# Kernel optimization log

Hardware: AMD Instinct MI355X
Metric: run time of the kernel (lower is better)

Reference implementation:

```python
import jax, jax.numpy as jnp
import numpy as np


def _conv2d_valid(x, w):
    # x: (N, C, H, W), w: (O, C, kH, kW) -> (N, O, H-kH+1, W-kW+1)
    return jax.lax.conv_general_dilated(
        x, w, window_strides=(1, 1), padding='VALID',
        dimension_numbers=('NCHW', 'OIHW', 'NCHW'))


def setup_inputs() -> dict:
    key = jax.random.key(0)
    kx, ky = jax.random.split(key)
    x = jax.random.normal(kx, (16, 64, 128, 128), dtype=jnp.float32)
    y = jax.random.normal(ky, (64, 64, 16, 16), dtype=jnp.float32)
    return {"x": x, "y": y}


def reference(x, y):
    # Normalize each of the K kernels to unit L2 norm (sum over C, kH, kW).
    normed_y = y / jnp.sqrt(jnp.sum(y * y, axis=(1, 2, 3), keepdims=True))
    # Per-window L2 norm of x via ones-kernel box conv over x^2.
    ones_kernel = jnp.ones(y.shape, dtype=x.dtype)
    x_norm = jnp.sqrt(_conv2d_valid(x * x, ones_kernel))
    # Normalized cross-correlation, clamped at zero.
    diss = _conv2d_valid(x, normed_y) / x_norm
    return jax.nn.relu(diss)
```

## Files before the change

### kernel.cpp

```cpp
#include <hip/hip_runtime.h>
#include <stdint.h>

#define GAS __attribute__((address_space(1)))
#define LAS __attribute__((address_space(3)))

typedef __attribute__((ext_vector_type(8))) short short8;
typedef __attribute__((ext_vector_type(4))) float float4v;
typedef __attribute__((ext_vector_type(4))) unsigned int uint4v;

__device__ __forceinline__ unsigned short f2bf(float f) {
  union { float f; unsigned int u; } v; v.f = f;
  unsigned int r = v.u + 0x7fffu + ((v.u >> 16) & 1u);
  return (unsigned short)(r >> 16);
}

__device__ __forceinline__ void async_g2l16(const void* g, void* l) {
  __builtin_amdgcn_global_load_lds((const GAS unsigned int*)g,
                                   (LAS unsigned int*)l, 16, 0, 0);
}

__device__ __forceinline__ void vmem_drain() {
  asm volatile("s_waitcnt vmcnt(0)" ::: "memory");
}

__global__ void knorm_y(const float* __restrict__ y, unsigned short* __restrict__ y_t2) {
  int o = blockIdx.x;
  int tid = threadIdx.x;
  const float* yo = y + o * 16384;
  float s = 0.f;
  for (int idx = tid; idx < 16384; idx += 256) { float v = yo[idx]; s += v * v; }
  for (int off = 32; off; off >>= 1) s += __shfl_down(s, off, 64);
  __shared__ float red[4];
  if ((tid & 63) == 0) red[tid >> 6] = s;
  __syncthreads();
  float rn = 1.0f / sqrtf(red[0] + red[1] + red[2] + red[3]);
  int og = o >> 4, ol = o & 15;
  for (int idx = tid; idx < 16384; idx += 256) {
    int c = idx >> 8, dy = (idx >> 4) & 15, dx = idx & 15;
    int t = dy * 16 + dx;
    int cb = c >> 5, q = (c >> 3) & 3, j = c & 7;
    size_t dst = (size_t)t * 4096 + (size_t)(og * 2 + cb) * 512 + (q * 16 + ol) * 8 + j;
    y_t2[dst] = f2bf(yo[idx] * rn);
  }
}

__global__ void ktrans_x(const float* __restrict__ x, unsigned short* __restrict__ x_t,
                         float* __restrict__ s) {
  int h = blockIdx.x, n = blockIdx.y;
  int tid = threadIdx.x;
  __shared__ __align__(16) unsigned short tb[8192];
  __shared__ float sb[256];
  const float* xb = x + ((size_t)n * 64) * 16384 + h * 128;
  int w = tid & 127, half = tid >> 7;
  float acc = 0.f;
#pragma unroll
  for (int cs = 0; cs < 4; ++cs) {
    short8 tmp;
#pragma unroll
    for (int j = 0; j < 8; ++j) {
      int c = half * 32 + cs * 8 + j;
      float v = xb[(size_t)c * 16384 + w];
      tmp[j] = (short)f2bf(v);
      acc += v * v;
    }
    int chunk = (half * 4 + cs) ^ (w & 7);
    *(short8*)(tb + w * 64 + chunk * 8) = tmp;
  }
  sb[tid] = acc;
  __syncthreads();
  uint4v* dst = (uint4v*)(x_t + ((size_t)(n * 128 + h)) * 8192);
  const uint4v* src = (const uint4v*)tb;
  for (int idx = tid; idx < 1024; idx += 256) dst[idx] = src[idx];
  if (tid < 128) s[((size_t)(n * 128 + h)) * 128 + tid] = sb[tid] + sb[tid + 128];
}

__global__ void knorm_x(const float* __restrict__ s, float* __restrict__ invn) {
  int i = blockIdx.x, n = blockIdx.y;
  int tid = threadIdx.x;
  __shared__ float colsum[128];
  const float* sp = s + ((size_t)(n * 128 + i)) * 128;
  float a = 0.f;
#pragma unroll
  for (int dy = 0; dy < 16; ++dy) a += sp[dy * 128 + tid];
  colsum[tid] = a;
  __syncthreads();
  if (tid < 113) {
    float acc = 0.f;
#pragma unroll
    for (int dx = 0; dx < 16; ++dx) acc += colsum[tid + dx];
    invn[((size_t)n * 113 + i) * 113 + tid] = 1.0f / sqrtf(acc);
  }
}

__launch_bounds__(256, 3)
__global__ void kconv(const unsigned short* __restrict__ x_t,
                      const unsigned short* __restrict__ y_t2,
                      const float* __restrict__ invn,
                      float* __restrict__ out) {
  int i = blockIdx.x;
  int n = blockIdx.y;
  int tid = threadIdx.x;
  int lane = tid & 63, wave = tid >> 6;
  int lane15 = lane & 15, q = lane >> 4;
  int wrow = wave >> 1, wcol = wave & 1;

  __shared__ __align__(16) char smem[32768];
  char* const A0 = smem;
  char* const A1 = smem + 16384;

  const char* xrow0 = (const char*)(x_t + ((size_t)(n * 128 + i)) * 8192);

  auto stageA = [&](int dy, char* buf) {
    const char* src = xrow0 + (size_t)dy * 16384;
#pragma unroll
    for (int it = 0; it < 4; ++it) {
      int chunk = it * 256 + wave * 64;
      async_g2l16(src + (chunk + lane) * 16, buf + chunk * 16);
    }
  };

  const short8* ybase = (const short8*)(y_t2 + (size_t)wcol * 2048 + (size_t)lane * 8);
  auto loadB = [&](int t, short8 bf[2][2]) {
    const short8* p = ybase + (size_t)t * 512;
    bf[0][0] = p[0];
    bf[0][1] = p[64];
    bf[1][0] = p[128];
    bf[1][1] = p[192];
  };

  float4v acc[4][2];
#pragma unroll
  for (int mt = 0; mt < 4; ++mt)
#pragma unroll
    for (int nt = 0; nt < 2; ++nt) acc[mt][nt] = (float4v){0.f, 0.f, 0.f, 0.f};

  int abase[4];
#pragma unroll
  for (int mt = 0; mt < 4; ++mt) abase[mt] = (wrow * 64 + mt * 16 + lane15) * 128;

  stageA(0, A0);
  short8 bc[2][2];
  loadB(0, bc);
  vmem_drain();
  __syncthreads();

#pragma unroll 1
  for (int dy = 0; dy < 16; ++dy) {
    char* Ab = (dy & 1) ? A1 : A0;
    if (dy < 15) stageA(dy + 1, (dy & 1) ? A0 : A1);
#pragma unroll
    for (int dx = 0; dx < 16; ++dx) {
      int t = dy * 16 + dx;
      short8 bn[2][2];
      if (t < 255) loadB(t + 1, bn);
      int xr = (lane15 + dx) & 7;
#pragma unroll
      for (int cb = 0; cb < 2; ++cb) {
        int aoff = dx * 128 + (((q + cb * 4) ^ xr) << 4);
#pragma unroll
        for (int mt = 0; mt < 4; ++mt) {
          short8 a = *(const short8*)(Ab + abase[mt] + aoff);
          acc[mt][0] = __builtin_amdgcn_mfma_f32_16x16x32_bf16(a, bc[0][cb], acc[mt][0], 0, 0, 0);
          acc[mt][1] = __builtin_amdgcn_mfma_f32_16x16x32_bf16(a, bc[1][cb], acc[mt][1], 0, 0, 0);
        }
      }
      if (t < 255) {
        bc[0][0] = bn[0][0]; bc[0][1] = bn[0][1];
        bc[1][0] = bn[1][0]; bc[1][1] = bn[1][1];
      }
    }
    vmem_drain();
    __syncthreads();
  }

  float* cs = (float*)smem;
  float* ivs = cs + 4352;
  const float* ivp = invn + ((size_t)n * 113 + i) * 113;
  if (tid < 128) ivs[tid] = (tid < 113) ? ivp[tid] : 0.f;
  float* op = out + (size_t)n * 64 * 12769 + (size_t)i * 113;
#pragma unroll 1
  for (int p = 0; p < 2; ++p) {
    if (wcol == p) {
#pragma unroll
      for (int mt = 0; mt < 4; ++mt)
#pragma unroll
        for (int nt = 0; nt < 2; ++nt) {
          int row = nt * 16 + lane15;
          int j0 = wrow * 64 + mt * 16 + q * 4;
          *(float4v*)(cs + row * 132 + j0) = acc[mt][nt];
        }
    }
    __syncthreads();
    for (int idx = tid; idx < 4096; idx += 256) {
      int o2 = idx >> 7, j = idx & 127;
      if (j < 113) {
        float v = cs[o2 * 132 + j] * ivs[j];
        op[(size_t)(p * 32 + o2) * 12769 + j] = fmaxf(v, 0.f);
      }
    }
    __syncthreads();
  }
}

extern "C" void kernel_launch(void* const* d_in, const int* in_sizes, int n_in,
                              void* d_out, int out_size, void* d_ws, size_t ws_size,
                              hipStream_t stream) {
  const float* x = (const float*)d_in[0];
  const float* y = (const float*)d_in[1];
  float* out = (float*)d_out;
  char* ws = (char*)d_ws;
  unsigned short* x_t = (unsigned short*)ws;
  unsigned short* y_t2 = (unsigned short*)(ws + 33554432);
  float* s = (float*)(ws + 35651584);
  float* invn = (float*)(ws + 36700160);

  hipLaunchKernelGGL(knorm_y, dim3(64), dim3(256), 0, stream, y, y_t2);
  hipLaunchKernelGGL(ktrans_x, dim3(128, 16), dim3(256), 0, stream, x, x_t, s);
  hipLaunchKernelGGL(knorm_x, dim3(113, 16), dim3(128), 0, stream, s, invn);
  hipLaunchKernelGGL(kconv, dim3(113, 16), dim3(256), 0, stream, x_t, y_t2, invn, out);
}
```

Before: 546.5 us.

## Use two waves per block each computing 64x64 tile in conv kernel

The conv kernel drops from four waves in a 2x2 layout to two waves, each covering all 64 output channels for its 64 output columns. Each A fragment read from LDS now feeds four MFMAs instead of two, halving LDS reads per MFMA, and the duplicated per-wave B loads are removed. In exchange each wave holds twice the accumulators and B registers, and the block has fewer waves to hide latency. Staging and the epilogue are adjusted to match the 128-thread block.

```diff
diff --git a/kernel.cpp b/kernel.cpp
--- a/kernel.cpp
+++ b/kernel.cpp
@@ -92,7 +92,7 @@
   }
 }
 
-__launch_bounds__(256, 3)
+__launch_bounds__(128, 2)
 __global__ void kconv(const unsigned short* __restrict__ x_t,
                       const unsigned short* __restrict__ y_t2,
                       const float* __restrict__ invn,
@@ -102,7 +102,6 @@
   int tid = threadIdx.x;
   int lane = tid & 63, wave = tid >> 6;
   int lane15 = lane & 15, q = lane >> 4;
-  int wrow = wave >> 1, wcol = wave & 1;
 
   __shared__ __align__(16) char smem[32768];
   char* const A0 = smem;
@@ -113,33 +112,33 @@
   auto stageA = [&](int dy, char* buf) {
     const char* src = xrow0 + (size_t)dy * 16384;
 #pragma unroll
-    for (int it = 0; it < 4; ++it) {
-      int chunk = it * 256 + wave * 64;
+    for (int it = 0; it < 8; ++it) {
+      int chunk = it * 128 + wave * 64;
       async_g2l16(src + (chunk + lane) * 16, buf + chunk * 16);
     }
   };
 
-  const short8* ybase = (const short8*)(y_t2 + (size_t)wcol * 2048 + (size_t)lane * 8);
-  auto loadB = [&](int t, short8 bf[2][2]) {
+  const short8* ybase = (const short8*)y_t2 + lane;
+  auto loadB = [&](int t, short8 bf[4][2]) {
     const short8* p = ybase + (size_t)t * 512;
-    bf[0][0] = p[0];
-    bf[0][1] = p[64];
-    bf[1][0] = p[128];
-    bf[1][1] = p[192];
+#pragma unroll
+    for (int nt = 0; nt < 4; ++nt)
+#pragma unroll
+      for (int cb = 0; cb < 2; ++cb) bf[nt][cb] = p[(nt * 2 + cb) * 64];
   };
 
-  float4v acc[4][2];
+  float4v acc[4][4];
 #pragma unroll
   for (int mt = 0; mt < 4; ++mt)
 #pragma unroll
-    for (int nt = 0; nt < 2; ++nt) acc[mt][nt] = (float4v){0.f, 0.f, 0.f, 0.f};
+    for (int nt = 0; nt < 4; ++nt) acc[mt][nt] = (float4v){0.f, 0.f, 0.f, 0.f};
 
   int abase[4];
 #pragma unroll
-  for (int mt = 0; mt < 4; ++mt) abase[mt] = (wrow * 64 + mt * 16 + lane15) * 128;
+  for (int mt = 0; mt < 4; ++mt) abase[mt] = (wave * 64 + mt * 16 + lane15) * 128;
 
   stageA(0, A0);
-  short8 bc[2][2];
+  short8 bc[4][2];
   loadB(0, bc);
   vmem_drain();
   __syncthreads();
@@ -151,7 +150,7 @@
 #pragma unroll
     for (int dx = 0; dx < 16; ++dx) {
       int t = dy * 16 + dx;
-      short8 bn[2][2];
+      short8 bn[4][2];
       if (t < 255) loadB(t + 1, bn);
       int xr = (lane15 + dx) & 7;
 #pragma unroll
@@ -160,13 +159,16 @@
 #pragma unroll
         for (int mt = 0; mt < 4; ++mt) {
           short8 a = *(const short8*)(Ab + abase[mt] + aoff);
-          acc[mt][0] = __builtin_amdgcn_mfma_f32_16x16x32_bf16(a, bc[0][cb], acc[mt][0], 0, 0, 0);
-          acc[mt][1] = __builtin_amdgcn_mfma_f32_16x16x32_bf16(a, bc[1][cb], acc[mt][1], 0, 0, 0);
+#pragma unroll
+          for (int nt = 0; nt < 4; ++nt)
+            acc[mt][nt] = __builtin_amdgcn_mfma_f32_16x16x32_bf16(a, bc[nt][cb], acc[mt][nt], 0, 0, 0);
         }
       }
       if (t < 255) {
-        bc[0][0] = bn[0][0]; bc[0][1] = bn[0][1];
-        bc[1][0] = bn[1][0]; bc[1][1] = bn[1][1];
+#pragma unroll
+        for (int nt = 0; nt < 4; ++nt)
+#pragma unroll
+          for (int cb = 0; cb < 2; ++cb) bc[nt][cb] = bn[nt][cb];
       }
     }
     vmem_drain();
@@ -174,24 +176,23 @@
   }
 
   float* cs = (float*)smem;
-  float* ivs = cs + 4352;
+  float* ivs = cs + 4224;
   const float* ivp = invn + ((size_t)n * 113 + i) * 113;
-  if (tid < 128) ivs[tid] = (tid < 113) ? ivp[tid] : 0.f;
+  ivs[tid] = (tid < 113) ? ivp[tid] : 0.f;
   float* op = out + (size_t)n * 64 * 12769 + (size_t)i * 113;
 #pragma unroll 1
   for (int p = 0; p < 2; ++p) {
-    if (wcol == p) {
-#pragma unroll
-      for (int mt = 0; mt < 4; ++mt)
-#pragma unroll
-        for (int nt = 0; nt < 2; ++nt) {
-          int row = nt * 16 + lane15;
-          int j0 = wrow * 64 + mt * 16 + q * 4;
-          *(float4v*)(cs + row * 132 + j0) = acc[mt][nt];
-        }
-    }
+#pragma unroll
+    for (int mt = 0; mt < 4; ++mt)
+#pragma unroll
+      for (int ntl = 0; ntl < 2; ++ntl) {
+        int nt = p * 2 + ntl;
+        int row = ntl * 16 + lane15;
+        int j0 = wave * 64 + mt * 16 + q * 4;
+        *(float4v*)(cs + row * 132 + j0) = acc[mt][nt];
+      }
     __syncthreads();
-    for (int idx = tid; idx < 4096; idx += 256) {
+    for (int idx = tid; idx < 4096; idx += 128) {
       int o2 = idx >> 7, j = idx & 127;
       if (j < 113) {
         float v = cs[o2 * 132 + j] * ivs[j];
@@ -217,5 +218,5 @@
   hipLaunchKernelGGL(knorm_y, dim3(64), dim3(256), 0, stream, y, y_t2);
   hipLaunchKernelGGL(ktrans_x, dim3(128, 16), dim3(256), 0, stream, x, x_t, s);
   hipLaunchKernelGGL(knorm_x, dim3(113, 16), dim3(128), 0, stream, s, invn);
-  hipLaunchKernelGGL(kconv, dim3(113, 16), dim3(256), 0, stream, x_t, y_t2, invn, out);
-}
+  hipLaunchKernelGGL(kconv, dim3(113, 16), dim3(128), 0, stream, x_t, y_t2, invn, out);
+}
```

Result: slower. 1.694 ms (+210.0%).
